# Kernel optimization log

Hardware: AMD Instinct MI355X
Metric: run time of the kernel (lower is better)

The kernel has to match this reference:

```python
import jax, jax.numpy as jnp
import numpy as np
import math

DIM = 768
HEADS = 8
DIM_HEAD = 64
INNER = HEADS * DIM_HEAD  # 512
B, L = 2, 4096
LN_EPS = 1e-5


def setup_inputs() -> dict:
    key = jax.random.key(0)
    ks = jax.random.split(key, 6)
    std = 0.02
    return {
        "x": jax.random.normal(ks[0], (B, L, DIM), dtype=jnp.float32),
        "ln_gamma": jnp.ones((DIM,), dtype=jnp.float32),
        "ln_beta": jnp.zeros((DIM,), dtype=jnp.float32),
        "Wq": jax.random.normal(ks[1], (DIM, INNER), dtype=jnp.float32) * std,
        "Wkv": jax.random.normal(ks[2], (DIM, 2 * INNER), dtype=jnp.float32) * std,
        "Wo": jax.random.normal(ks[3], (INNER, DIM), dtype=jnp.float32) * std,
    }


def reference(x, ln_gamma, ln_beta, Wq, Wkv, Wo):
    b, l, _ = x.shape
    # LayerNorm (eps=1e-5, affine)
    mu = jnp.mean(x, axis=-1, keepdims=True)
    var = jnp.mean(jnp.square(x - mu), axis=-1, keepdims=True)
    xn = (x - mu) * jax.lax.rsqrt(var + LN_EPS) * ln_gamma + ln_beta

    q = xn @ Wq                      # (b, l, inner)
    kv = xn @ Wkv                    # (b, l, 2*inner)
    k, v = jnp.split(kv, 2, axis=-1)

    def to_heads(t):
        return t.reshape(b, l, HEADS, DIM_HEAD).transpose(0, 2, 1, 3)  # (b,h,l,d)

    q, k, v = to_heads(q), to_heads(k), to_heads(v)

    scale = 1.0 / math.sqrt(math.sqrt(DIM_HEAD))
    # explicit quadratic scores, softmax in float32 as in original
    weight = jnp.einsum("bhid,bhjd->bhij", q * scale, k * scale)
    weight = jax.nn.softmax(weight.astype(jnp.float32), axis=-1).astype(q.dtype)
    out = jnp.einsum("bhij,bhjd->bhid", weight, v)       # (b,h,l,d)
    out = out.transpose(0, 2, 1, 3).reshape(b, l, INNER)  # merge heads
    return out @ Wo
```

## Files before the change

kernel.cpp:

```cpp
#include <hip/hip_runtime.h>
#include <hip/hip_bf16.h>


typedef __bf16 bf16_t;
typedef __bf16 bf16x4 __attribute__((ext_vector_type(4)));
typedef __bf16 bf16x8 __attribute__((ext_vector_type(8)));
typedef float f32x4 __attribute__((ext_vector_type(4)));

#define MFMA16(a, b, c) __builtin_amdgcn_mfma_f32_16x16x32_bf16((a), (b), (c), 0, 0, 0)

#define QSCALE 0.18033688011112042f

#define GLDS(gp, lp)                                                          \
    __builtin_amdgcn_global_load_lds(                                         \
        (const __attribute__((address_space(1))) void*)(gp),                  \
        (__attribute__((address_space(3))) void*)(lp), 16, 0, 0)

__global__ void detect_kernel(const unsigned int* __restrict__ xw, int* __restrict__ flag) {
    const int i = threadIdx.x;
    int cnt = 0;
#pragma unroll
    for (int j = 0; j < 2; ++j) {
        const unsigned int e = (xw[i * 2 + j] >> 7) & 0xFF;
        cnt += (e >= 100 && e <= 140) ? 1 : 0;
    }
#pragma unroll
    for (int off = 1; off < 64; off <<= 1) cnt += __shfl_xor(cnt, off, 64);
    if (i == 0) *flag = (cnt < 64) ? 1 : 0;
}

__global__ __launch_bounds__(256) void ln_kernel(const void* __restrict__ xv,
                                                 const void* __restrict__ gv,
                                                 const void* __restrict__ bv,
                                                 bf16_t* __restrict__ xn,
                                                 const int* __restrict__ flag) {
    const int f32 = *flag;
    const int row = blockIdx.x;
    const int t = threadIdx.x;

    float v[3];
    if (f32) {
        const float* xr = (const float*)xv + (size_t)row * 768;
#pragma unroll
        for (int i = 0; i < 3; ++i) v[i] = xr[t + i * 256];
    } else {
        const bf16_t* xr = (const bf16_t*)xv + (size_t)row * 768;
#pragma unroll
        for (int i = 0; i < 3; ++i) v[i] = (float)xr[t + i * 256];
    }
    float s = v[0] + v[1] + v[2];
    float sq = v[0] * v[0] + v[1] * v[1] + v[2] * v[2];
#pragma unroll
    for (int off = 1; off < 64; off <<= 1) {
        s += __shfl_xor(s, off, 64);
        sq += __shfl_xor(sq, off, 64);
    }
    __shared__ float red[8];
    const int w = t >> 6, lane = t & 63;
    if (lane == 0) { red[w] = s; red[4 + w] = sq; }
    __syncthreads();
    const float S = red[0] + red[1] + red[2] + red[3];
    const float SQ = red[4] + red[5] + red[6] + red[7];
    const float mu = S * (1.0f / 768.0f);
    const float var = SQ * (1.0f / 768.0f) - mu * mu;
    const float rstd = rsqrtf(var + 1e-5f);

    bf16_t* xo = xn + (size_t)row * 768;
#pragma unroll
    for (int i = 0; i < 3; ++i) {
        const int c = t + i * 256;
        const float gc = f32 ? ((const float*)gv)[c] : (float)((const bf16_t*)gv)[c];
        const float bc = f32 ? ((const float*)bv)[c] : (float)((const bf16_t*)bv)[c];
        xo[c] = (bf16_t)(((v[i] - mu) * rstd) * gc + bc);
    }
}

__global__ __launch_bounds__(256) void transpose_w(const void* __restrict__ in,
                                                   bf16_t* __restrict__ out,
                                                   int R, int C,
                                                   const int* __restrict__ flag) {
    const int f32 = *flag;
    const int idx = blockIdx.x * 256 + threadIdx.x;
    if (idx < R * C) {
        const int r = idx / C, c = idx % C;
        const float val = f32 ? ((const float*)in)[idx] : (float)((const bf16_t*)in)[idx];
        out[(size_t)c * R + r] = (bf16_t)val;
    }
}

__global__ __launch_bounds__(256) void gemm_bt(const bf16_t* __restrict__ A,
                                               const bf16_t* __restrict__ BT,
                                               void* __restrict__ C,
                                               int M, int N, int K,
                                               const int* __restrict__ out_flag) {
    const int m0 = blockIdx.y * 128;
    const int n0 = blockIdx.x * 128;
    __shared__ bf16_t As[128 * 32];
    __shared__ bf16_t Bs[128 * 32];

    const int t = threadIdx.x;
    const int lane = t & 63;
    const int w = t >> 6;
    const int wm = (w >> 1) * 64;
    const int wn = (w & 1) * 64;
    const int quad = lane >> 4;
    const int cl = lane & 15;

    f32x4 acc[4][4];
    const f32x4 z4 = {0.f, 0.f, 0.f, 0.f};
#pragma unroll
    for (int mi = 0; mi < 4; ++mi)
#pragma unroll
        for (int ni = 0; ni < 4; ++ni) acc[mi][ni] = z4;

    const int r0 = lane >> 2;
    const int c0 = (lane & 3) * 8;
    const bf16_t* AgL = A + (size_t)(m0 + w * 32 + r0) * K + c0;
    const bf16_t* AgH = A + (size_t)(m0 + w * 32 + 16 + r0) * K + c0;
    const bf16_t* BgL = BT + (size_t)(n0 + w * 32 + r0) * K + c0;
    const bf16_t* BgH = BT + (size_t)(n0 + w * 32 + 16 + r0) * K + c0;
    bf16_t* AdL = &As[(w * 32) * 32];
    bf16_t* AdH = &As[(w * 32 + 16) * 32];
    bf16_t* BdL = &Bs[(w * 32) * 32];
    bf16_t* BdH = &Bs[(w * 32 + 16) * 32];

    for (int kt = 0; kt < K; kt += 32) {
        __syncthreads();
        GLDS(AgL + kt, AdL);
        GLDS(AgH + kt, AdH);
        GLDS(BgL + kt, BdL);
        GLDS(BgH + kt, BdH);
        __syncthreads();

        const int ko = quad * 8;
        bf16x8 af[4], bfr[4];
#pragma unroll
        for (int mi = 0; mi < 4; ++mi)
            af[mi] = *(const bf16x8*)&As[(wm + mi * 16 + cl) * 32 + ko];
#pragma unroll
        for (int ni = 0; ni < 4; ++ni)
            bfr[ni] = *(const bf16x8*)&Bs[(wn + ni * 16 + cl) * 32 + ko];
#pragma unroll
        for (int mi = 0; mi < 4; ++mi)
#pragma unroll
            for (int ni = 0; ni < 4; ++ni)
                acc[mi][ni] = MFMA16(af[mi], bfr[ni], acc[mi][ni]);
    }

    const int f32out = (out_flag != nullptr) && (*out_flag != 0);
#pragma unroll
    for (int mi = 0; mi < 4; ++mi) {
#pragma unroll
        for (int ni = 0; ni < 4; ++ni) {
#pragma unroll
            for (int r4 = 0; r4 < 4; ++r4) {
                const int row = m0 + wm + mi * 16 + quad * 4 + r4;
                const int col = n0 + wn + ni * 16 + cl;
                if (f32out)
                    ((float*)C)[(size_t)row * N + col] = acc[mi][ni][r4];
                else
                    ((bf16_t*)C)[(size_t)row * N + col] = (bf16_t)acc[mi][ni][r4];
            }
        }
    }
}

__global__ __launch_bounds__(256) void vtrans(const bf16_t* __restrict__ qkv,
                                              bf16_t* __restrict__ vtg) {
    const int tt = blockIdx.x;
    const int bh = blockIdx.y;
    const int b = bh >> 3, h = bh & 7;
    const int tok0 = tt * 64;
    __shared__ bf16_t Ts[64 * 68];
    const int t = threadIdx.x;
    {
        const int r = t >> 2, c = (t & 3) * 16;
        const bf16_t* src = qkv + ((size_t)b * 4096 + tok0 + r) * 1536 + 1024 + h * 64 + c;
        *(bf16x8*)&Ts[r * 68 + c] = *(const bf16x8*)src;
        *(bf16x8*)&Ts[r * 68 + c + 8] = *(const bf16x8*)(src + 8);
    }
    __syncthreads();
    {
        const int d = t >> 2, seg = (t & 3) * 16;
        bf16x8 v0, v1;
#pragma unroll
        for (int j = 0; j < 8; ++j) v0[j] = Ts[(seg + j) * 68 + d];
#pragma unroll
        for (int j = 0; j < 8; ++j) v1[j] = Ts[(seg + 8 + j) * 68 + d];
        bf16_t* dst = vtg + ((size_t)bh * 64 + d) * 4096 + tok0 + seg;
        *(bf16x8*)dst = v0;
        *(bf16x8*)(dst + 8) = v1;
    }
}

__global__ __launch_bounds__(256, 2) void attn_kernel(const bf16_t* __restrict__ qkv,
                                                      const bf16_t* __restrict__ vtg,
                                                      bf16_t* __restrict__ ao) {
    const int qt = blockIdx.x;
    const int bh = blockIdx.y;
    const int b = bh >> 3, h = bh & 7;
    const int q0 = qt * 128;

    __shared__ bf16_t Ps[4][64 * 68];
    __shared__ bf16_t Ks[2][64 * 68];
    __shared__ bf16_t Vs[2][64 * 68];

    const int t = threadIdx.x;
    const int lane = t & 63;
    const int w = t >> 6;
    const int qsub = w & 1;
    const int kh = w >> 1;
    const int quad = lane >> 4;
    const int cl = lane & 15;

    const size_t rowbase = (size_t)b * 4096;
    const int qcol = h * 64;
    const int kcol = 512 + h * 64;

    {
        const int r = t >> 1;
        const int half = (t & 1) * 32;
        const bf16_t* src = qkv + (rowbase + q0 + r) * 1536 + qcol + half;
#pragma unroll
        for (int o8 = 0; o8 < 4; ++o8) {
            bf16x8 v = *(const bf16x8*)(src + o8 * 8);
#pragma unroll
            for (int e = 0; e < 8; ++e) v[e] = (bf16_t)((float)v[e] * QSCALE);
            *(bf16x8*)&Ps[0][r * 68 + half + o8 * 8] = v;
        }
    }
    __syncthreads();

    bf16x8 aq[4][2];
#pragma unroll
    for (int rt = 0; rt < 4; ++rt)
#pragma unroll
        for (int hh = 0; hh < 2; ++hh)
            aq[rt][hh] = *(const bf16x8*)&Ps[0][(qsub * 64 + rt * 16 + cl) * 68 +
                                               hh * 32 + quad * 8];

    bf16x8 ones;
#pragma unroll
    for (int e = 0; e < 8; ++e) ones[e] = (bf16_t)1.0f;

    const f32x4 z4 = {0.f, 0.f, 0.f, 0.f};
    f32x4 o[4][4];
    f32x4 l_acc[4];
#pragma unroll
    for (int rt = 0; rt < 4; ++rt) {
        l_acc[rt] = z4;
#pragma unroll
        for (int ni = 0; ni < 4; ++ni) o[rt][ni] = z4;
    }

    const int t2 = qsub * 64 + lane;
    const int sr = t2 >> 1;
    const int sh = (t2 & 1) * 32;

    bf16x8 kreg[4], vreg[4];
    {
        const int k0 = kh * 2048;
        const bf16_t* ks = qkv + (rowbase + k0 + sr) * 1536 + kcol + sh;
        const bf16_t* vs = vtg + ((size_t)bh * 64 + sr) * 4096 + k0 + sh;
#pragma unroll
        for (int o8 = 0; o8 < 4; ++o8) {
            kreg[o8] = *(const bf16x8*)(ks + o8 * 8);
            vreg[o8] = *(const bf16x8*)(vs + o8 * 8);
        }
    }

    for (int it = 0; it < 32; ++it) {
        __syncthreads();
#pragma unroll
        for (int o8 = 0; o8 < 4; ++o8) {
            *(bf16x8*)&Ks[kh][sr * 68 + sh + o8 * 8] = kreg[o8];
            *(bf16x8*)&Vs[kh][sr * 68 + sh + o8 * 8] = vreg[o8];
        }
        __syncthreads();

        if (it < 31) {
            const int k0n = kh * 2048 + (it + 1) * 64;
            const bf16_t* ks = qkv + (rowbase + k0n + sr) * 1536 + kcol + sh;
            const bf16_t* vs = vtg + ((size_t)bh * 64 + sr) * 4096 + k0n + sh;
#pragma unroll
            for (int o8 = 0; o8 < 4; ++o8) {
                kreg[o8] = *(const bf16x8*)(ks + o8 * 8);
                vreg[o8] = *(const bf16x8*)(vs + o8 * 8);
            }
        }

        const int ko = quad * 8;
        bf16x8 kb[4][2];
#pragma unroll
        for (int ni = 0; ni < 4; ++ni) {
            kb[ni][0] = *(const bf16x8*)&Ks[kh][(ni * 16 + cl) * 68 + ko];
            kb[ni][1] = *(const bf16x8*)&Ks[kh][(ni * 16 + cl) * 68 + 32 + ko];
        }
#pragma unroll
        for (int rt = 0; rt < 4; ++rt) {
#pragma unroll
            for (int ni = 0; ni < 4; ++ni) {
                f32x4 s = z4;
                s = MFMA16(kb[ni][0], aq[rt][0], s);
                s = MFMA16(kb[ni][1], aq[rt][1], s);
                bf16x4 pk;
#pragma unroll
                for (int r4 = 0; r4 < 4; ++r4) pk[r4] = (bf16_t)exp2f(s[r4]);
                *(bf16x4*)&Ps[w][(rt * 16 + cl) * 68 + ni * 16 + quad * 4] = pk;
            }
        }

        bf16x8 vb[4][2];
#pragma unroll
        for (int ni = 0; ni < 4; ++ni) {
            vb[ni][0] = *(const bf16x8*)&Vs[kh][(ni * 16 + cl) * 68 + ko];
            vb[ni][1] = *(const bf16x8*)&Vs[kh][(ni * 16 + cl) * 68 + 32 + ko];
        }
#pragma unroll
        for (int rt = 0; rt < 4; ++rt) {
            const bf16x8 p0 = *(const bf16x8*)&Ps[w][(rt * 16 + cl) * 68 + ko];
            const bf16x8 p1 = *(const bf16x8*)&Ps[w][(rt * 16 + cl) * 68 + 32 + ko];
#pragma unroll
            for (int ni = 0; ni < 4; ++ni) {
                o[rt][ni] = MFMA16(p0, vb[ni][0], o[rt][ni]);
                o[rt][ni] = MFMA16(p1, vb[ni][1], o[rt][ni]);
            }
            l_acc[rt] = MFMA16(p0, ones, l_acc[rt]);
            l_acc[rt] = MFMA16(p1, ones, l_acc[rt]);
        }
    }

    float* cb = (float*)&Ps[0][0];
    __syncthreads();
    if (kh == 1) {
#pragma unroll
        for (int rt = 0; rt < 4; ++rt) {
#pragma unroll
            for (int r4 = 0; r4 < 4; ++r4) {
                const int row = rt * 16 + quad * 4 + r4;
                float* rp = cb + qsub * 4160 + row * 65;
#pragma unroll
                for (int ni = 0; ni < 4; ++ni) rp[ni * 16 + cl] = o[rt][ni][r4];
                if (cl == 0) rp[64] = l_acc[rt][r4];
            }
        }
    }
    __syncthreads();
    if (kh == 0) {
#pragma unroll
        for (int rt = 0; rt < 4; ++rt) {
#pragma unroll
            for (int r4 = 0; r4 < 4; ++r4) {
                const int row = rt * 16 + quad * 4 + r4;
                const float* rp = cb + qsub * 4160 + row * 65;
                const float inv = 1.0f / (l_acc[rt][r4] + rp[64]);
                const size_t orow = rowbase + q0 + qsub * 64 + row;
#pragma unroll
                for (int ni = 0; ni < 4; ++ni)
                    ao[orow * 512 + h * 64 + ni * 16 + cl] =
                        (bf16_t)((o[rt][ni][r4] + rp[ni * 16 + cl]) * inv);
            }
        }
    }
}

extern "C" void kernel_launch(void* const* d_in, const int* in_sizes, int n_in,
                              void* d_out, int out_size, void* d_ws, size_t ws_size,
                              hipStream_t stream) {
    const void* x = d_in[0];
    const void* gamma = d_in[1];
    const void* beta = d_in[2];
    const void* Wq = d_in[3];
    const void* Wkv = d_in[4];
    const void* Wo = d_in[5];

    char* wsb = (char*)d_ws;
    int* flag = (int*)wsb;
    bf16_t* xn = (bf16_t*)(wsb + 256);
    bf16_t* WqkvT = xn + (size_t)8192 * 768;
    bf16_t* WoT = WqkvT + (size_t)1536 * 768;
    bf16_t* qkv = WoT + (size_t)768 * 512;
    bf16_t* aob = xn;
    bf16_t* vtg = (bf16_t*)d_out;

    detect_kernel<<<1, 64, 0, stream>>>((const unsigned int*)x, flag);

    ln_kernel<<<8192, 256, 0, stream>>>(x, gamma, beta, xn, flag);

    transpose_w<<<(768 * 512 + 255) / 256, 256, 0, stream>>>(Wq, WqkvT, 768, 512, flag);
    transpose_w<<<(768 * 1024 + 255) / 256, 256, 0, stream>>>(
        Wkv, WqkvT + (size_t)512 * 768, 768, 1024, flag);
    transpose_w<<<(512 * 768 + 255) / 256, 256, 0, stream>>>(Wo, WoT, 512, 768, flag);

    gemm_bt<<<dim3(12, 64), 256, 0, stream>>>(xn, WqkvT, (void*)qkv, 8192, 1536, 768,
                                              nullptr);

    vtrans<<<dim3(64, 16), 256, 0, stream>>>(qkv, vtg);

    attn_kernel<<<dim3(32, 16), 256, 0, stream>>>(qkv, vtg, aob);

    gemm_bt<<<dim3(6, 64), 256, 0, stream>>>(aob, WoT, d_out, 8192, 768, 512, flag);
}
```

Before: 274.1 us.

## Vectorize LayerNorm, tile weight transposes via LDS, add 128x64 output GEMM

LayerNorm now handles one row per wave with vectorized 12-element loads and stores, which removes the cross-wave shared-memory reduction and barrier. The weight transposes go from scattered per-element writes to a 64x64 LDS-tiled transpose with coalesced 16-byte reads and writes. The output projection moves to a new 128x64-tile, 128-thread GEMM, doubling the block count to 768 so more CUs are busy. Each block now gets less reuse per load, and the output GEMM's epilogue still writes scalar values.

```diff
diff --git a/kernel.cpp b/kernel.cpp
--- a/kernel.cpp
+++ b/kernel.cpp
@@ -35,43 +35,51 @@
                                                  bf16_t* __restrict__ xn,
                                                  const int* __restrict__ flag) {
     const int f32 = *flag;
-    const int row = blockIdx.x;
-    const int t = threadIdx.x;
-
-    float v[3];
+    const int lane = threadIdx.x & 63;
+    const int row = blockIdx.x * 4 + (threadIdx.x >> 6);
+    const int c0 = lane * 12;
+
+    float v[12];
     if (f32) {
-        const float* xr = (const float*)xv + (size_t)row * 768;
-#pragma unroll
-        for (int i = 0; i < 3; ++i) v[i] = xr[t + i * 256];
+        const float* xr = (const float*)xv + (size_t)row * 768 + c0;
+#pragma unroll
+        for (int i = 0; i < 3; ++i) {
+            const float4 q = *(const float4*)(xr + i * 4);
+            v[i * 4] = q.x; v[i * 4 + 1] = q.y; v[i * 4 + 2] = q.z; v[i * 4 + 3] = q.w;
+        }
     } else {
-        const bf16_t* xr = (const bf16_t*)xv + (size_t)row * 768;
-#pragma unroll
-        for (int i = 0; i < 3; ++i) v[i] = (float)xr[t + i * 256];
-    }
-    float s = v[0] + v[1] + v[2];
-    float sq = v[0] * v[0] + v[1] * v[1] + v[2] * v[2];
+        const bf16_t* xr = (const bf16_t*)xv + (size_t)row * 768 + c0;
+#pragma unroll
+        for (int i = 0; i < 3; ++i) {
+            const bf16x4 q = *(const bf16x4*)(xr + i * 4);
+#pragma unroll
+            for (int j = 0; j < 4; ++j) v[i * 4 + j] = (float)q[j];
+        }
+    }
+    float s = 0.f, sq = 0.f;
+#pragma unroll
+    for (int j = 0; j < 12; ++j) { s += v[j]; sq += v[j] * v[j]; }
 #pragma unroll
     for (int off = 1; off < 64; off <<= 1) {
         s += __shfl_xor(s, off, 64);
         sq += __shfl_xor(sq, off, 64);
     }
-    __shared__ float red[8];
-    const int w = t >> 6, lane = t & 63;
-    if (lane == 0) { red[w] = s; red[4 + w] = sq; }
-    __syncthreads();
-    const float S = red[0] + red[1] + red[2] + red[3];
-    const float SQ = red[4] + red[5] + red[6] + red[7];
-    const float mu = S * (1.0f / 768.0f);
-    const float var = SQ * (1.0f / 768.0f) - mu * mu;
+    const float mu = s * (1.0f / 768.0f);
+    const float var = sq * (1.0f / 768.0f) - mu * mu;
     const float rstd = rsqrtf(var + 1e-5f);
 
-    bf16_t* xo = xn + (size_t)row * 768;
+    bf16_t* xo = xn + (size_t)row * 768 + c0;
 #pragma unroll
     for (int i = 0; i < 3; ++i) {
-        const int c = t + i * 256;
-        const float gc = f32 ? ((const float*)gv)[c] : (float)((const bf16_t*)gv)[c];
-        const float bc = f32 ? ((const float*)bv)[c] : (float)((const bf16_t*)bv)[c];
-        xo[c] = (bf16_t)(((v[i] - mu) * rstd) * gc + bc);
+        bf16x4 o;
+#pragma unroll
+        for (int j = 0; j < 4; ++j) {
+            const int c = c0 + i * 4 + j;
+            const float gc = f32 ? ((const float*)gv)[c] : (float)((const bf16_t*)gv)[c];
+            const float bc = f32 ? ((const float*)bv)[c] : (float)((const bf16_t*)bv)[c];
+            o[j] = (bf16_t)((v[i * 4 + j] - mu) * rstd * gc + bc);
+        }
+        *(bf16x4*)(xo + i * 4) = o;
     }
 }
 
@@ -80,11 +88,38 @@
                                                    int R, int C,
                                                    const int* __restrict__ flag) {
     const int f32 = *flag;
-    const int idx = blockIdx.x * 256 + threadIdx.x;
-    if (idx < R * C) {
-        const int r = idx / C, c = idx % C;
-        const float val = f32 ? ((const float*)in)[idx] : (float)((const bf16_t*)in)[idx];
-        out[(size_t)c * R + r] = (bf16_t)val;
+    __shared__ bf16_t Ts[64 * 68];
+    const int r0 = blockIdx.y * 64, c0 = blockIdx.x * 64;
+    const int t = threadIdx.x;
+    {
+        const int r = t >> 2, c = (t & 3) * 16;
+        if (f32) {
+            const float* src = (const float*)in + (size_t)(r0 + r) * C + c0 + c;
+#pragma unroll
+            for (int i = 0; i < 16; i += 4) {
+                const float4 q = *(const float4*)(src + i);
+                Ts[r * 68 + c + i] = (bf16_t)q.x;
+                Ts[r * 68 + c + i + 1] = (bf16_t)q.y;
+                Ts[r * 68 + c + i + 2] = (bf16_t)q.z;
+                Ts[r * 68 + c + i + 3] = (bf16_t)q.w;
+            }
+        } else {
+            const bf16_t* src = (const bf16_t*)in + (size_t)(r0 + r) * C + c0 + c;
+            *(bf16x8*)&Ts[r * 68 + c] = *(const bf16x8*)src;
+            *(bf16x8*)&Ts[r * 68 + c + 8] = *(const bf16x8*)(src + 8);
+        }
+    }
+    __syncthreads();
+    {
+        const int oc = t >> 2, seg = (t & 3) * 16;
+        bf16x8 v0, v1;
+#pragma unroll
+        for (int j = 0; j < 8; ++j) v0[j] = Ts[(seg + j) * 68 + oc];
+#pragma unroll
+        for (int j = 0; j < 8; ++j) v1[j] = Ts[(seg + 8 + j) * 68 + oc];
+        bf16_t* dst = out + (size_t)(c0 + oc) * R + r0 + seg;
+        *(bf16x8*)dst = v0;
+        *(bf16x8*)(dst + 8) = v1;
     }
 }
 
@@ -156,6 +191,77 @@
             for (int r4 = 0; r4 < 4; ++r4) {
                 const int row = m0 + wm + mi * 16 + quad * 4 + r4;
                 const int col = n0 + wn + ni * 16 + cl;
+                if (f32out)
+                    ((float*)C)[(size_t)row * N + col] = acc[mi][ni][r4];
+                else
+                    ((bf16_t*)C)[(size_t)row * N + col] = (bf16_t)acc[mi][ni][r4];
+            }
+        }
+    }
+}
+
+__global__ __launch_bounds__(128) void gemm_bt64(const bf16_t* __restrict__ A,
+                                                 const bf16_t* __restrict__ BT,
+                                                 void* __restrict__ C,
+                                                 int M, int N, int K,
+                                                 const int* __restrict__ out_flag) {
+    const int m0 = blockIdx.y * 128;
+    const int n0 = blockIdx.x * 64;
+    __shared__ bf16_t As[128 * 32];
+    __shared__ bf16_t Bs[64 * 32];
+
+    const int t = threadIdx.x;
+    const int lane = t & 63;
+    const int w = t >> 6;
+    const int quad = lane >> 4;
+    const int cl = lane & 15;
+
+    f32x4 acc[4][4];
+    const f32x4 z4 = {0.f, 0.f, 0.f, 0.f};
+#pragma unroll
+    for (int mi = 0; mi < 4; ++mi)
+#pragma unroll
+        for (int ni = 0; ni < 4; ++ni) acc[mi][ni] = z4;
+
+    const int r0 = lane >> 2;
+    const int c0 = (lane & 3) * 8;
+    const bf16_t* Ag = A + (size_t)(m0 + w * 64 + r0) * K + c0;
+    const bf16_t* Bg = BT + (size_t)(n0 + w * 32 + r0) * K + c0;
+    bf16_t* Ad = &As[(w * 64) * 32];
+    bf16_t* Bd = &Bs[(w * 32) * 32];
+
+    for (int kt = 0; kt < K; kt += 32) {
+        __syncthreads();
+#pragma unroll
+        for (int i = 0; i < 4; ++i) GLDS(Ag + kt + (size_t)i * 16 * K, Ad + i * 512);
+#pragma unroll
+        for (int i = 0; i < 2; ++i) GLDS(Bg + kt + (size_t)i * 16 * K, Bd + i * 512);
+        __syncthreads();
+
+        const int ko = quad * 8;
+        bf16x8 af[4], bfr[4];
+#pragma unroll
+        for (int mi = 0; mi < 4; ++mi)
+            af[mi] = *(const bf16x8*)&As[(w * 64 + mi * 16 + cl) * 32 + ko];
+#pragma unroll
+        for (int ni = 0; ni < 4; ++ni)
+            bfr[ni] = *(const bf16x8*)&Bs[(ni * 16 + cl) * 32 + ko];
+#pragma unroll
+        for (int mi = 0; mi < 4; ++mi)
+#pragma unroll
+            for (int ni = 0; ni < 4; ++ni)
+                acc[mi][ni] = MFMA16(af[mi], bfr[ni], acc[mi][ni]);
+    }
+
+    const int f32out = (out_flag != nullptr) && (*out_flag != 0);
+#pragma unroll
+    for (int mi = 0; mi < 4; ++mi) {
+#pragma unroll
+        for (int ni = 0; ni < 4; ++ni) {
+#pragma unroll
+            for (int r4 = 0; r4 < 4; ++r4) {
+                const int row = m0 + w * 64 + mi * 16 + quad * 4 + r4;
+                const int col = n0 + ni * 16 + cl;
                 if (f32out)
                     ((float*)C)[(size_t)row * N + col] = acc[mi][ni][r4];
                 else
@@ -385,12 +491,12 @@
 
     detect_kernel<<<1, 64, 0, stream>>>((const unsigned int*)x, flag);
 
-    ln_kernel<<<8192, 256, 0, stream>>>(x, gamma, beta, xn, flag);
-
-    transpose_w<<<(768 * 512 + 255) / 256, 256, 0, stream>>>(Wq, WqkvT, 768, 512, flag);
-    transpose_w<<<(768 * 1024 + 255) / 256, 256, 0, stream>>>(
-        Wkv, WqkvT + (size_t)512 * 768, 768, 1024, flag);
-    transpose_w<<<(512 * 768 + 255) / 256, 256, 0, stream>>>(Wo, WoT, 512, 768, flag);
+    ln_kernel<<<2048, 256, 0, stream>>>(x, gamma, beta, xn, flag);
+
+    transpose_w<<<dim3(8, 12), 256, 0, stream>>>(Wq, WqkvT, 768, 512, flag);
+    transpose_w<<<dim3(16, 12), 256, 0, stream>>>(Wkv, WqkvT + (size_t)512 * 768, 768,
+                                                  1024, flag);
+    transpose_w<<<dim3(12, 8), 256, 0, stream>>>(Wo, WoT, 512, 768, flag);
 
     gemm_bt<<<dim3(12, 64), 256, 0, stream>>>(xn, WqkvT, (void*)qkv, 8192, 1536, 768,
                                               nullptr);
@@ -399,5 +505,5 @@
 
     attn_kernel<<<dim3(32, 16), 256, 0, stream>>>(qkv, vtg, aob);
 
-    gemm_bt<<<dim3(6, 64), 256, 0, stream>>>(aob, WoT, d_out, 8192, 768, 512, flag);
-}
+    gemm_bt64<<<dim3(12, 64), 128, 0, stream>>>(aob, WoT, d_out, 8192, 768, 512, flag);
+}
```

Result: no change. 274.1 us (-0.0%).
